# Optimization experiments

Hardware: AMD Instinct MI355X
Metric: run time of the kernel (lower is better)

The kernel has to match this reference:

```python
import jax, jax.numpy as jnp
import numpy as np

# dims matching init_kwargs / input_specs
B, C, H = 8, 256, 48          # input (B, C, H, H)
GRID = 3                       # sqrt(num_memory)
NUM_MEM = GRID * GRID          # 9
WS = H // GRID                 # window_size = 16
S = 128                        # num_slots
D = WS * WS * C                # slot_dim = 65536
K = 5                          # gumbel top-k threshold (shrink_thres, int)
EPS = 1e-12


def setup_inputs() -> dict:
    key = jax.random.key(0)
    k1, k2, k3 = jax.random.split(key, 3)
    stdv = 1.0 / np.sqrt(D)
    x = jax.random.normal(k1, (B, C, H, H), dtype=jnp.float32)
    mem1 = jax.random.uniform(k2, (NUM_MEM, S, D), jnp.float32, -stdv, stdv)
    mem2 = jax.random.uniform(k3, (NUM_MEM, S, D), jnp.float32, -stdv, stdv)
    return {"x": x, "mem1": mem1, "mem2": mem2}


def _window_partition(x):
    # (B, C, H, W) -> (B, NUM_MEM, WS*WS*C); per-window layout is (ws, ws, C) row-major,
    # matching torch unfold -> view(B,C,ws^2,L) -> permute(0,3,2,1).
    b = x.shape[0]
    x = jnp.transpose(x, (0, 2, 3, 1))                        # (B, H, W, C)
    x = x.reshape(b, GRID, WS, GRID, WS, C)
    x = jnp.transpose(x, (0, 1, 3, 2, 4, 5))                  # (B, gh, gw, ws, ws, C)
    return x.reshape(b, NUM_MEM, WS * WS * C)


def _window_reverse(w):
    # (B, NUM_MEM, WS*WS*C) -> (B, C, H, W); exact inverse of _window_partition.
    b = w.shape[0]
    w = w.reshape(b, GRID, GRID, WS, WS, C)
    w = jnp.transpose(w, (0, 1, 3, 2, 4, 5)).reshape(b, H, H, C)
    return jnp.transpose(w, (0, 3, 1, 2))


def _hard_shrink_relu(y, lambd):
    d = y - lambd
    return jax.nn.relu(d) * y / (jnp.abs(d) + EPS)


def _memory_read(q, mem):
    # q: (B, M, D) window queries; mem: (M, S, D) per-window memory matrices.
    att = jnp.einsum('bmd,msd->bms', q, mem)                  # (B, M, S)
    y = jax.nn.softmax(att, axis=-1)
    k = min(S - 1, K)
    thres = jax.lax.top_k(y, k)[0][..., -1:]                  # kth largest per row
    y_hard = _hard_shrink_relu(y, thres)
    y_hard = y_hard / jnp.maximum(jnp.sum(jnp.abs(y_hard), axis=-1, keepdims=True), EPS)
    y_hard = jax.lax.stop_gradient(y_hard - y) + y            # straight-through
    return jnp.einsum('bms,msd->bmd', y_hard, mem)            # (B, M, D)


def reference(x, mem1, mem2):
    # CRU modeled as identity split: x1 = x2 = x (CRU source not provided).
    q = _window_partition(x)                                  # (B, 9, D)
    out1 = _window_reverse(_memory_read(q, mem1))
    out2 = _window_reverse(_memory_read(q, mem2))
    return out1 + out2                                        # eval mode: no bernoulli mask
```

## Files before the change

### kernel.cpp

```cpp
#include <hip/hip_runtime.h>
#include <hip/hip_bf16.h>
#include <cstdint>

#define Bn 8
#define Cn 256
#define Hn 48
#define NUM_MEM 9
#define WSZ 16
#define Sn 128
#define Dn 65536
#define KTOP 5
#define ND 128
#define CH 512

__global__ __launch_bounds__(256) void k_x2q(const float* __restrict__ x,
                                             float* __restrict__ q) {
    const int h = blockIdx.x;
    const int b = blockIdx.y;
    const int gh = h >> 4, i = h & 15;
    __shared__ float tile[Cn * Hn];
    const float* xp = x + (size_t)b * Cn * Hn * Hn + (size_t)h * Hn;
    for (int o = threadIdx.x; o < Cn * Hn; o += blockDim.x) {
        int c = o / Hn, w = o - c * Hn;
        tile[o] = xp[(size_t)c * Hn * Hn + w];
    }
    __syncthreads();
    for (int gw = 0; gw < 3; ++gw) {
        float* qp = q + (size_t)(b * NUM_MEM + gh * 3 + gw) * Dn + i * (WSZ * Cn);
        for (int l = threadIdx.x; l < WSZ * Cn; l += blockDim.x) {
            int j = l >> 8, c = l & 255;
            qp[l] = tile[c * Hn + gw * WSZ + j];
        }
    }
}

__global__ __launch_bounds__(256) void k_att2(const float* __restrict__ q,
                                              const float* __restrict__ mem1,
                                              const float* __restrict__ mem2,
                                              float* __restrict__ ap) {
    const int dc = blockIdx.x;
    const int mw = blockIdx.y;
    const int e  = blockIdx.z;
    const float4* mem4 = (const float4*)(e ? mem2 : mem1);
    const float4* q4   = (const float4*)q;
    const int lane = threadIdx.x & 63, wave = threadIdx.x >> 6;

    float4 qr[8][2];
#pragma unroll
    for (int b = 0; b < 8; ++b) {
        const size_t qb = (size_t)(b * NUM_MEM + mw) * (Dn / 4) + (size_t)dc * (CH / 4);
        qr[b][0] = q4[qb + lane];
        qr[b][1] = q4[qb + 64 + lane];
    }

    const float4* mrow = mem4 + (size_t)(mw * Sn + wave) * (Dn / 4) + (size_t)dc * (CH / 4) + lane;
    float4 Mv0 = mrow[0], Mv1 = mrow[64];

    for (int s = wave; s < Sn; s += 4) {
        const float4* nrow = (s + 4 < Sn) ? (mrow + Dn) : mrow;
        float4 Mn0 = nrow[0], Mn1 = nrow[64];

        float a[8];
#pragma unroll
        for (int b = 0; b < 8; ++b) {
            a[b] = qr[b][0].x * Mv0.x + qr[b][0].y * Mv0.y + qr[b][0].z * Mv0.z + qr[b][0].w * Mv0.w
                 + qr[b][1].x * Mv1.x + qr[b][1].y * Mv1.y + qr[b][1].z * Mv1.z + qr[b][1].w * Mv1.w;
        }

#pragma unroll
        for (int i = 0; i < 3; ++i) {
            const int mk = 1 << i;
            const bool up = (lane & mk) != 0;
#pragma unroll
            for (int j = 0; j < (8 >> (i + 1)); ++j) {
                float lo = a[2 * j], hi = a[2 * j + 1];
                float mine = up ? hi : lo;
                float th   = __shfl_xor(up ? lo : hi, mk, 64);
                a[j] = mine + th;
            }
        }
        float r = a[0];
#pragma unroll
        for (int off = 8; off < 64; off <<= 1) r += __shfl_xor(r, off, 64);
        if (lane < 8)
            ap[((size_t)dc * 144 + (size_t)(e * 8 + lane) * 9 + mw) * Sn + s] = r;

        Mv0 = Mn0; Mv1 = Mn1;
        mrow += Dn;
    }
}

__global__ __launch_bounds__(128) void k_smax(const float* __restrict__ ap,
                                              float* __restrict__ w) {
    const int row = blockIdx.x;
    const int t = threadIdx.x;
    __shared__ float sf[Sn];
    __shared__ unsigned long long sk[Sn];

    float v = 0.f;
#pragma unroll 8
    for (int nd = 0; nd < ND; ++nd)
        v += ap[((size_t)nd * 144 + row) * Sn + t];

    sf[t] = v; __syncthreads();
    for (int s = 64; s > 0; s >>= 1) { if (t < s) sf[t] = fmaxf(sf[t], sf[t + s]); __syncthreads(); }
    float mx = sf[0]; __syncthreads();

    float e = expf(v - mx);
    sf[t] = e; __syncthreads();
    for (int s = 64; s > 0; s >>= 1) { if (t < s) sf[t] += sf[t + s]; __syncthreads(); }
    float sum = sf[0]; __syncthreads();
    float y = e / sum;

    bool alive = true;
    float thres = 0.f;
    unsigned int ybits = __float_as_uint(y);
    for (int it = 0; it < KTOP; ++it) {
        sk[t] = alive ? ((((unsigned long long)ybits) << 32) | (unsigned)t) : 0ull;
        __syncthreads();
        for (int s = 64; s > 0; s >>= 1) {
            if (t < s) { if (sk[t + s] > sk[t]) sk[t] = sk[t + s]; }
            __syncthreads();
        }
        unsigned long long kmax = sk[0];
        __syncthreads();
        if ((unsigned)(kmax & 0xffffffffull) == (unsigned)t) alive = false;
        thres = __uint_as_float((unsigned)(kmax >> 32));
    }

    float d   = y - thres;
    float num = fmaxf(d, 0.f) * y;
    float yh  = num / (fabsf(d) + 1e-12f);

    sf[t] = yh; __syncthreads();
    for (int s = 64; s > 0; s >>= 1) { if (t < s) sf[t] += sf[t + s]; __syncthreads(); }
    float l1 = sf[0];
    w[(size_t)row * Sn + t] = yh / fmaxf(l1, 1e-12f);
}

__global__ __launch_bounds__(256) void k_acc(const float* __restrict__ w,
                                             const float* __restrict__ mem1,
                                             const float* __restrict__ mem2,
                                             float* __restrict__ acc) {
    const int chunk = blockIdx.x;
    const int m     = blockIdx.y;
    const int b     = blockIdx.z;
    __shared__ int   nz[2];
    __shared__ int   idx[2][16];
    __shared__ float wv[2][16];
    if (threadIdx.x < 2) nz[threadIdx.x] = 0;
    __syncthreads();
    {
        int eidx = threadIdx.x >> 7;
        int s    = threadIdx.x & 127;
        float ww = w[((size_t)(eidx * Bn + b) * NUM_MEM + m) * Sn + s];
        if (ww != 0.f) {
            int p = atomicAdd(&nz[eidx], 1);
            if (p < 16) { idx[eidx][p] = s; wv[eidx][p] = ww; }
        }
    }
    __syncthreads();
    const int n1 = nz[0], n2 = nz[1];
    const size_t mbase = (size_t)m * Sn * Dn;
    const int dbase = chunk * 4096;
    for (int l = threadIdx.x * 4; l < 4096; l += 1024) {
        int d = dbase + l;
        float4 a = {0.f, 0.f, 0.f, 0.f};
        for (int j = 0; j < n1; ++j) {
            const float4 r = *(const float4*)(mem1 + mbase + (size_t)idx[0][j] * Dn + d);
            float ww = wv[0][j];
            a.x += ww * r.x; a.y += ww * r.y; a.z += ww * r.z; a.w += ww * r.w;
        }
        for (int j = 0; j < n2; ++j) {
            const float4 r = *(const float4*)(mem2 + mbase + (size_t)idx[1][j] * Dn + d);
            float ww = wv[1][j];
            a.x += ww * r.x; a.y += ww * r.y; a.z += ww * r.z; a.w += ww * r.w;
        }
        *(float4*)(acc + (size_t)(b * NUM_MEM + m) * Dn + d) = a;
    }
}

__global__ __launch_bounds__(256) void k_q2x(const float* __restrict__ acc,
                                             float* __restrict__ out) {
    const int h = blockIdx.x;
    const int b = blockIdx.y;
    const int gh = h >> 4, i = h & 15;
    __shared__ float tile[Cn * Hn];
    for (int gw = 0; gw < 3; ++gw) {
        const float* ap = acc + (size_t)(b * NUM_MEM + gh * 3 + gw) * Dn + i * (WSZ * Cn);
        for (int l = threadIdx.x; l < WSZ * Cn; l += blockDim.x) {
            int j = l >> 8, c = l & 255;
            tile[c * Hn + gw * WSZ + j] = ap[l];
        }
    }
    __syncthreads();
    float* op = out + (size_t)b * Cn * Hn * Hn + (size_t)h * Hn;
    for (int o = threadIdx.x; o < Cn * Hn; o += blockDim.x) {
        int c = o / Hn, wcol = o - c * Hn;
        op[(size_t)c * Hn * Hn + wcol] = tile[o];
    }
}

extern "C" void kernel_launch(void* const* d_in, const int* in_sizes, int n_in,
                              void* d_out, int out_size, void* d_ws, size_t ws_size,
                              hipStream_t stream) {
    const float* x    = (const float*)d_in[0];
    const float* mem1 = (const float*)d_in[1];
    const float* mem2 = (const float*)d_in[2];
    float* out = (float*)d_out;

    float* q    = (float*)d_ws;
    float* wbuf = q + (size_t)Bn * NUM_MEM * Dn;
    float* ap   = (float*)d_out;

    k_x2q<<<dim3(Hn, Bn), 256, 0, stream>>>(x, q);
    k_att2<<<dim3(ND, NUM_MEM, 2), 256, 0, stream>>>(q, mem1, mem2, ap);
    k_smax<<<2 * Bn * NUM_MEM, 128, 0, stream>>>(ap, wbuf);
    k_acc<<<dim3(16, NUM_MEM, Bn), 256, 0, stream>>>(wbuf, mem1, mem2, q );
    k_q2x<<<dim3(Hn, Bn), 256, 0, stream>>>(q, out);
}
```

Before: 233.9 us.

## Retile attention kernel to register-block 4 slots by 8 batches

Rewrites the attention dot-product kernel so each wave computes a 4-slot by 8-batch register tile over a 4096-element D segment, accumulating across 16 steps before one shuffle-based transpose-reduction. This replaces the old per-slot reduction done after every 512-element chunk, cutting shuffle overhead and shrinking the partial-sum buffer from 128 to 16 D-splits, so the softmax kernel sums fewer partials. The cost is more registers per thread (32 accumulators plus 24 float4 values in flight) and heavier q reloads, since q is now re-read per slot group instead of kept resident.

```diff
diff --git a/kernel.cpp b/kernel.cpp
--- a/kernel.cpp
+++ b/kernel.cpp
@@ -10,8 +10,7 @@
 #define Sn 128
 #define Dn 65536
 #define KTOP 5
-#define ND 128
-#define CH 512
+#define ND2 16
 
 __global__ __launch_bounds__(256) void k_x2q(const float* __restrict__ x,
                                              float* __restrict__ q) {
@@ -34,59 +33,78 @@
     }
 }
 
-__global__ __launch_bounds__(256) void k_att2(const float* __restrict__ q,
+__global__ __launch_bounds__(256) void k_att3(const float* __restrict__ q,
                                               const float* __restrict__ mem1,
                                               const float* __restrict__ mem2,
                                               float* __restrict__ ap) {
-    const int dc = blockIdx.x;
-    const int mw = blockIdx.y;
-    const int e  = blockIdx.z;
+    const int dseg = blockIdx.x;
+    const int mw   = blockIdx.y;
+    const int sgrp = blockIdx.z;
+    const int e    = sgrp >> 3;
+    const int lane = threadIdx.x & 63, wave = threadIdx.x >> 6;
+    const int s0   = (sgrp & 7) * 16 + wave * 4;
+
     const float4* mem4 = (const float4*)(e ? mem2 : mem1);
     const float4* q4   = (const float4*)q;
-    const int lane = threadIdx.x & 63, wave = threadIdx.x >> 6;
-
-    float4 qr[8][2];
-#pragma unroll
-    for (int b = 0; b < 8; ++b) {
-        const size_t qb = (size_t)(b * NUM_MEM + mw) * (Dn / 4) + (size_t)dc * (CH / 4);
-        qr[b][0] = q4[qb + lane];
-        qr[b][1] = q4[qb + 64 + lane];
-    }
-
-    const float4* mrow = mem4 + (size_t)(mw * Sn + wave) * (Dn / 4) + (size_t)dc * (CH / 4) + lane;
-    float4 Mv0 = mrow[0], Mv1 = mrow[64];
-
-    for (int s = wave; s < Sn; s += 4) {
-        const float4* nrow = (s + 4 < Sn) ? (mrow + Dn) : mrow;
-        float4 Mn0 = nrow[0], Mn1 = nrow[64];
-
-        float a[8];
-#pragma unroll
-        for (int b = 0; b < 8; ++b) {
-            a[b] = qr[b][0].x * Mv0.x + qr[b][0].y * Mv0.y + qr[b][0].z * Mv0.z + qr[b][0].w * Mv0.w
-                 + qr[b][1].x * Mv1.x + qr[b][1].y * Mv1.y + qr[b][1].z * Mv1.z + qr[b][1].w * Mv1.w;
-        }
-
-#pragma unroll
-        for (int i = 0; i < 3; ++i) {
-            const int mk = 1 << i;
-            const bool up = (lane & mk) != 0;
-#pragma unroll
-            for (int j = 0; j < (8 >> (i + 1)); ++j) {
-                float lo = a[2 * j], hi = a[2 * j + 1];
-                float mine = up ? hi : lo;
-                float th   = __shfl_xor(up ? lo : hi, mk, 64);
-                a[j] = mine + th;
+
+    const int off0 = dseg * 1024 + lane;
+    const float4* mr[4];
+    const float4* qr[8];
+#pragma unroll
+    for (int r = 0; r < 4; ++r)
+        mr[r] = mem4 + (size_t)(mw * Sn + s0 + r) * (Dn / 4) + off0;
+#pragma unroll
+    for (int b = 0; b < 8; ++b)
+        qr[b] = q4 + (size_t)(b * NUM_MEM + mw) * (Dn / 4) + off0;
+
+    float a[32];
+#pragma unroll
+    for (int i = 0; i < 32; ++i) a[i] = 0.f;
+
+    float4 M[4], Q[8];
+#pragma unroll
+    for (int r = 0; r < 4; ++r) M[r] = mr[r][0];
+#pragma unroll
+    for (int b = 0; b < 8; ++b) Q[b] = qr[b][0];
+
+    for (int step = 0; step < 16; ++step) {
+        const int noff = (step < 15 ? step + 1 : step) * 64;
+        float4 Mn[4], Qn[8];
+#pragma unroll
+        for (int r = 0; r < 4; ++r) Mn[r] = mr[r][noff];
+#pragma unroll
+        for (int b = 0; b < 8; ++b) Qn[b] = qr[b][noff];
+
+#pragma unroll
+        for (int r = 0; r < 4; ++r)
+#pragma unroll
+            for (int b = 0; b < 8; ++b) {
+                a[r * 8 + b] += M[r].x * Q[b].x + M[r].y * Q[b].y
+                              + M[r].z * Q[b].z + M[r].w * Q[b].w;
             }
-        }
-        float r = a[0];
-#pragma unroll
-        for (int off = 8; off < 64; off <<= 1) r += __shfl_xor(r, off, 64);
-        if (lane < 8)
-            ap[((size_t)dc * 144 + (size_t)(e * 8 + lane) * 9 + mw) * Sn + s] = r;
-
-        Mv0 = Mn0; Mv1 = Mn1;
-        mrow += Dn;
+#pragma unroll
+        for (int r = 0; r < 4; ++r) M[r] = Mn[r];
+#pragma unroll
+        for (int b = 0; b < 8; ++b) Q[b] = Qn[b];
+    }
+
+#pragma unroll
+    for (int k = 0; k < 5; ++k) {
+        const int mk = 1 << k;
+        const bool up = (lane & mk) != 0;
+#pragma unroll
+        for (int j = 0; j < (32 >> (k + 1)); ++j) {
+            float lo = a[2 * j], hi = a[2 * j + 1];
+            float mine = up ? hi : lo;
+            float oth  = __shfl_xor(up ? lo : hi, mk, 64);
+            a[j] = mine + oth;
+        }
+    }
+    float rsum = a[0] + __shfl_xor(a[0], 32, 64);
+    if (lane < 32) {
+        const int b = lane & 7, r = (lane >> 3) & 3;
+        const int s = s0 + r;
+        ap[((size_t)dseg * 144 + (size_t)(e * 8 + b) * 9 + mw) * Sn + s] = rsum;
     }
 }
 
@@ -98,8 +116,8 @@
     __shared__ unsigned long long sk[Sn];
 
     float v = 0.f;
-#pragma unroll 8
-    for (int nd = 0; nd < ND; ++nd)
+#pragma unroll
+    for (int nd = 0; nd < ND2; ++nd)
         v += ap[((size_t)nd * 144 + row) * Sn + t];
 
     sf[t] = v; __syncthreads();
@@ -214,7 +232,7 @@
     float* ap   = (float*)d_out;
 
     k_x2q<<<dim3(Hn, Bn), 256, 0, stream>>>(x, q);
-    k_att2<<<dim3(ND, NUM_MEM, 2), 256, 0, stream>>>(q, mem1, mem2, ap);
+    k_att3<<<dim3(ND2, NUM_MEM, 16), 256, 0, stream>>>(q, mem1, mem2, ap);
     k_smax<<<2 * Bn * NUM_MEM, 128, 0, stream>>>(ap, wbuf);
     k_acc<<<dim3(16, NUM_MEM, Bn), 256, 0, stream>>>(wbuf, mem1, mem2, q );
     k_q2x<<<dim3(Hn, Bn), 256, 0, stream>>>(q, out);
```

Measured after the change: 233.7 us. Within noise of the previous version (-0.1%).
